# Optimization experiments

Hardware: AMD Instinct MI355X
Metric: run time of the kernel (lower is better)

The kernel has to match this reference:

```python
import jax
import jax.numpy as jnp
from jax import lax
import numpy as np

INPUT_DIM = 784
HIDDEN_DIM = 1024
BATCH = 256
N_BINS = 10


def setup_inputs() -> dict:
    key = jax.random.key(0)
    k1, k2, k3, k4, k5 = jax.random.split(key, 5)
    # kaiming-normal-ish init scales (faithful in spirit; exact values irrelevant for math)
    W = jax.random.normal(k1, (HIDDEN_DIM, INPUT_DIM), dtype=jnp.float32) * np.sqrt(2.0 / INPUT_DIM)
    c = jnp.zeros((HIDDEN_DIM, 1), dtype=jnp.float32)
    V = jax.random.normal(k2, (INPUT_DIM, HIDDEN_DIM, N_BINS), dtype=jnp.float32) * np.sqrt(2.0 / N_BINS)
    b = jnp.zeros((INPUT_DIM, N_BINS), dtype=jnp.float32)
    x = jax.random.randint(k3, (BATCH, INPUT_DIM), 0, N_BINS, dtype=jnp.int32)
    return {"x": x, "W": W, "c": c, "V": V, "b": b}


def reference(x, W, c, V, b):
    # x: [B, D] int pixel bins; W: [H, D]; c: [H, 1]; V: [D, H, 10]; b: [D, 10]
    B = x.shape[0]
    xf = x.astype(jnp.float32)  # [B, D]
    a0 = jnp.broadcast_to(c[:, 0][None, :], (B, W.shape[0]))  # [B, H]

    def step(a, inp):
        Vi, bi, Wi, xi = inp  # Vi:[H,10], bi:[10], Wi:[H], xi:[B]
        h = jax.nn.sigmoid(a)                       # [B, H]
        p = jax.nn.softmax(h @ Vi + bi, axis=1)     # [B, 10]
        a = a + xi[:, None] * Wi[None, :]           # rank-1 update, matches x_i @ W[:,i].T
        return a, p

    _, p_seq = lax.scan(step, a0, (V, b, W.T, xf.T))  # p_seq: [D, B, 10]
    p_hat = jnp.transpose(p_seq, (1, 2, 0))            # [B, 10, D] == torch.stack(p_hat, dim=2)
    return p_hat
```

## Files before the change

kernel.cpp:

```cpp
#include <hip/hip_runtime.h>
#include <stdint.h>

#define D_DIM 784
#define H_DIM 1024
#define B_DIM 256
#define NBIN  10
#define G_CH  8
#define T_CH  98
#define BT    16
#define BF    2
#define LOG2E 1.4426950408889634f

#define PSCAN_BLKS 256
#define VPREP_BLKS D_DIM
#define WPREP_BLKS 208

typedef _Float16 half8_t  __attribute__((ext_vector_type(8)));
typedef __fp16   fp16x2_t __attribute__((ext_vector_type(2)));
typedef float    float4_t __attribute__((ext_vector_type(4)));

__global__ void k_prep2(const float* __restrict__ W, const float* __restrict__ V,
                        const float* __restrict__ c, const int* __restrict__ x,
                        _Float16* __restrict__ Wt2h, _Float16* __restrict__ VB,
                        _Float16* __restrict__ PA) {
    __shared__ __align__(16) float smem[5120];
    int tid = threadIdx.x;
    int bx  = blockIdx.x;

    if (bx < PSCAN_BLKS) {
        int b0 = (bx & 127) * BF;
        int hg = bx >> 7;
        int h0 = hg * 512 + tid * 2;
        float* xs0 = smem;
        float* xs1 = smem + D_DIM;
        for (int qq = tid; qq < BF * (D_DIM / 4); qq += 256) {
            int bb = qq / (D_DIM / 4), r = qq % (D_DIM / 4);
            int4 xi = ((const int4*)(x + (size_t)(b0 + bb) * D_DIM))[r];
            float4 xf = make_float4((float)xi.x, (float)xi.y, (float)xi.z, (float)xi.w);
            *((float4*)((bb ? xs1 : xs0) + r * 4)) = xf;
        }
        float c0 = c[h0], c1 = c[h0 + 1];
        float acc00 = c0, acc01 = c1;
        float acc10 = c0, acc11 = c1;
        __syncthreads();
        const float4* w0 = (const float4*)(W + (size_t)h0 * D_DIM);
        const float4* w1 = (const float4*)(W + (size_t)(h0 + 1) * D_DIM);
        uint* pa0 = (uint*)PA + (size_t)b0 * (H_DIM / 2) + (h0 >> 1);

        auto pstore = [&](int t_) {
            union { _Float16 hh[2]; uint u; } u0, u1;
            u0.hh[0] = (_Float16)(acc00 * LOG2E); u0.hh[1] = (_Float16)(acc01 * LOG2E);
            u1.hh[0] = (_Float16)(acc10 * LOG2E); u1.hh[1] = (_Float16)(acc11 * LOG2E);
            pa0[(size_t)t_ * (B_DIM * H_DIM / 2)] = u0.u;
            pa0[(size_t)t_ * (B_DIM * H_DIM / 2) + (H_DIM / 2)] = u1.u;
        };
        auto pfma = [&](float4 a0_, float4 a1_, float4 b0_, float4 b1_, int t_) {
            float4 x00 = *((const float4*)(xs0 + t_ * 8));
            float4 x01 = *((const float4*)(xs0 + t_ * 8 + 4));
            float4 x10 = *((const float4*)(xs1 + t_ * 8));
            float4 x11 = *((const float4*)(xs1 + t_ * 8 + 4));
            acc00 += x00.x*a0_.x + x00.y*a0_.y + x00.z*a0_.z + x00.w*a0_.w
                   + x01.x*a1_.x + x01.y*a1_.y + x01.z*a1_.z + x01.w*a1_.w;
            acc01 += x00.x*b0_.x + x00.y*b0_.y + x00.z*b0_.z + x00.w*b0_.w
                   + x01.x*b1_.x + x01.y*b1_.y + x01.z*b1_.z + x01.w*b1_.w;
            acc10 += x10.x*a0_.x + x10.y*a0_.y + x10.z*a0_.z + x10.w*a0_.w
                   + x11.x*a1_.x + x11.y*a1_.y + x11.z*a1_.z + x11.w*a1_.w;
            acc11 += x10.x*b0_.x + x10.y*b0_.y + x10.z*b0_.z + x10.w*b0_.w
                   + x11.x*b1_.x + x11.y*b1_.y + x11.z*b1_.z + x11.w*b1_.w;
        };

        float4 A0 = w0[0], A1 = w0[1], B0 = w1[0], B1 = w1[1];
        for (int t = 0; t < T_CH; ++t) {
            int tn = (t + 1 < T_CH) ? t + 1 : t;
            float4 nA0 = w0[tn * 2], nA1 = w0[tn * 2 + 1];
            float4 nB0 = w1[tn * 2], nB1 = w1[tn * 2 + 1];
            pstore(t);
            pfma(A0, A1, B0, B1, t);
            A0 = nA0; A1 = nA1; B0 = nB0; B1 = nB1;
        }
    } else if (bx < PSCAN_BLKS + VPREP_BLKS) {
        int i = bx - PSCAN_BLKS;
        const float4* src = (const float4*)(V + (size_t)i * H_DIM * NBIN);
        uint4* dst = (uint4*)VB + (size_t)i * 2048;
        #pragma unroll
        for (int p = 0; p < 2; ++p) {
            if (p) __syncthreads();
            #pragma unroll
            for (int qv = 0; qv < 5; ++qv) {
                float4 v = src[p * 1280 + qv * 256 + tid];
                *((float4*)&smem[(qv * 256 + tid) * 4]) = v;
            }
            __syncthreads();
            #pragma unroll
            for (int qv = 0; qv < 4; ++qv) {
                int pair = p * 1024 + qv * 256 + tid;
                int kk = pair >> 6, ll = pair & 63;
                int n = ll & 15, hb = kk * 32 + ((ll >> 4) & 3) * 8;
                union { _Float16 hh[8]; uint4 u; } o;
                #pragma unroll
                for (int jj = 0; jj < 8; ++jj)
                    o.hh[jj] = (_Float16)((n < NBIN) ? smem[(hb + jj) * NBIN + n - p * 5120] : 0.0f);
                dst[pair] = o.u;
            }
        }
    } else {
        int qw = bx - PSCAN_BLKS - VPREP_BLKS;
        int j0 = (qw % 13) * 64, h0 = (qw / 13) * 64;
        float (*t)[65] = (float(*)[65])smem;
        int tj = tid & 63, tr = tid >> 6;
        int j = j0 + tj;
        #pragma unroll
        for (int r = 0; r < 16; ++r) {
            int hh = tr * 16 + r;
            t[hh][tj] = (j < D_DIM) ? W[(size_t)(h0 + hh) * D_DIM + j] : 0.0f;
        }
        __syncthreads();
        #pragma unroll
        for (int r = 0; r < 16; ++r) {
            int jj = tr * 16 + r;
            int jo = j0 + jj;
            if (jo < D_DIM) Wt2h[(size_t)jo * H_DIM + h0 + tj] = (_Float16)(t[tj][jj] * LOG2E);
        }
    }
}

__global__ __launch_bounds__(256, 4)
void k_main(const _Float16* __restrict__ VB, const _Float16* __restrict__ Wt2h,
            const _Float16* __restrict__ PA, const int* __restrict__ x,
            const float* __restrict__ bias, float* __restrict__ out) {
    int bt  = blockIdx.x;
    int tc  = blockIdx.y;
    int tid = threadIdx.x;
    int w   = tid >> 6;
    int l   = tid & 63;
    int bl  = l & 15;
    int kg  = l >> 4;
    int bg  = bt * BT + bl;
    int i0  = tc * G_CH;

    __shared__ __align__(16) _Float16 wlds[G_CH][H_DIM];
    __shared__ float red[4][64][18];
    __shared__ float bs[G_CH][16];

    {
        int ii = tid >> 4, n = tid & 15;
        if (ii < G_CH) bs[ii][n] = (n < NBIN) ? bias[(size_t)(i0 + ii) * NBIN + n] : 0.0f;
    }
    {
        #pragma unroll
        for (int r = 0; r < G_CH; ++r) {
            uint2 v = ((const uint2*)(Wt2h + (size_t)(i0 + r) * H_DIM))[tid];
            *((uint2*)&wlds[r][tid * 4]) = v;
        }
    }
    float xvf[G_CH];
    {
        const int4* xp = (const int4*)(x + (size_t)bg * D_DIM + i0);
        int4 x0 = xp[0], x1 = xp[1];
        xvf[0] = (float)x0.x; xvf[1] = (float)x0.y; xvf[2] = (float)x0.z; xvf[3] = (float)x0.w;
        xvf[4] = (float)x1.x; xvf[5] = (float)x1.y; xvf[6] = (float)x1.z; xvf[7] = (float)x1.w;
    }
    float a[8][8];
    {
        const _Float16* src = PA + ((size_t)tc * B_DIM + bg) * H_DIM + w * 256 + kg * 8;
        #pragma unroll
        for (int m = 0; m < 8; ++m) {
            half8_t av = *((const half8_t*)(src + m * 32));
            #pragma unroll
            for (int j = 0; j < 8; ++j) a[m][j] = (float)av[j];
        }
    }

    const uint4* vp = (const uint4*)VB + ((size_t)i0 * 32 + w * 8) * 64 + l;
    uint4 vbuf[3];
    vbuf[0] = vp[0];
    vbuf[1] = vp[64];
    float4_t acc = {0.f, 0.f, 0.f, 0.f};

    auto step = [&](int mm) {
        const int ii = mm >> 3, m = mm & 7;
        if (mm + 2 < 64) {
            const int nn = mm + 2;
            vbuf[nn % 3] = vp[((nn >> 3) * 32 + (nn & 7)) * 64];
        }
        union { half8_t h8; uint u32[4]; } af;
        #pragma unroll
        for (int p = 0; p < 4; ++p) {
            float s0 = __builtin_amdgcn_rcpf(1.0f + __builtin_amdgcn_exp2f(-a[m][2 * p]));
            float s1 = __builtin_amdgcn_rcpf(1.0f + __builtin_amdgcn_exp2f(-a[m][2 * p + 1]));
            union { fp16x2_t v; uint u; } cv;
            cv.v = __builtin_amdgcn_cvt_pkrtz(s0, s1);
            af.u32[p] = cv.u;
        }
        union { half8_t h8; uint4 u; } bf;
        bf.u = vbuf[mm % 3];
        acc = __builtin_amdgcn_mfma_f32_16x16x32_f16(af.h8, bf.h8, acc, 0, 0, 0);
        half8_t wh = *((const half8_t*)&wlds[ii][w * 256 + kg * 8 + m * 32]);
        float xf = xvf[ii];
        a[m][0] += xf * (float)wh[0]; a[m][1] += xf * (float)wh[1];
        a[m][2] += xf * (float)wh[2]; a[m][3] += xf * (float)wh[3];
        a[m][4] += xf * (float)wh[4]; a[m][5] += xf * (float)wh[5];
        a[m][6] += xf * (float)wh[6]; a[m][7] += xf * (float)wh[7];
        if (m == 7) {
            int s = (ii & 3) * 4;
            red[w][l][s + 0] = acc[0]; red[w][l][s + 1] = acc[1];
            red[w][l][s + 2] = acc[2]; red[w][l][s + 3] = acc[3];
            acc = (float4_t){0.f, 0.f, 0.f, 0.f};
        }
    };

    auto softmax_store = [&](int half) {
        float p4[4];
        #pragma unroll
        for (int q = 0; q < 4; ++q) {
            int ii = half * 4 + q;
            float tot = red[0][l][q * 4 + w] + red[1][l][q * 4 + w]
                      + red[2][l][q * 4 + w] + red[3][l][q * 4 + w];
            float v = (bl < NBIN) ? tot + bs[ii][bl] : -3.0e38f;
            float vm = v;
            vm = fmaxf(vm, __shfl_xor(vm, 1));
            vm = fmaxf(vm, __shfl_xor(vm, 2));
            vm = fmaxf(vm, __shfl_xor(vm, 4));
            vm = fmaxf(vm, __shfl_xor(vm, 8));
            float e = __builtin_amdgcn_exp2f((v - vm) * LOG2E);
            float ss = e;
            ss += __shfl_xor(ss, 1); ss += __shfl_xor(ss, 2);
            ss += __shfl_xor(ss, 4); ss += __shfl_xor(ss, 8);
            p4[q] = e * __builtin_amdgcn_rcpf(ss);
        }
        if (bl < NBIN) {
            int b = bt * BT + kg * 4 + w;
            size_t base = ((size_t)b * NBIN + bl) * D_DIM + i0 + half * 4;
            float4 v = make_float4(p4[0], p4[1], p4[2], p4[3]);
            *((float4*)(out + base)) = v;
        }
    };

    __syncthreads();
    #pragma unroll
    for (int mm = 0; mm < 32; ++mm) step(mm);
    __syncthreads();
    softmax_store(0);
    __syncthreads();
    #pragma unroll
    for (int mm = 32; mm < 64; ++mm) step(mm);
    __syncthreads();
    softmax_store(1);
}

extern "C" void kernel_launch(void* const* d_in, const int* in_sizes, int n_in,
                              void* d_out, int out_size, void* d_ws, size_t ws_size,
                              hipStream_t stream) {
    const int*   x    = (const int*)d_in[0];
    const float* W    = (const float*)d_in[1];
    const float* c    = (const float*)d_in[2];
    const float* V    = (const float*)d_in[3];
    const float* bias = (const float*)d_in[4];
    float* out = (float*)d_out;

    char* ws = (char*)d_ws;
    size_t off = 0;
    _Float16* Wt2h = (_Float16*)(ws + off);
    off += (size_t)D_DIM * H_DIM * sizeof(_Float16);
    off = (off + 255) & ~(size_t)255;
    _Float16* VB = (_Float16*)(ws + off);
    off += (size_t)D_DIM * 32 * 64 * 8 * sizeof(_Float16);
    off = (off + 255) & ~(size_t)255;
    _Float16* PA = (_Float16*)(ws + off);

    k_prep2<<<dim3(PSCAN_BLKS + VPREP_BLKS + WPREP_BLKS), 256, 0, stream>>>(W, V, c, x, Wt2h, VB, PA);
    k_main<<<dim3(B_DIM / BT, T_CH), 256, 0, stream>>>(VB, Wt2h, PA, x, bias, out);
}
```

Measured before the change: 219.4 us.

## Split prefix-scan prep across time groups with four batch rows per block

The prefix-sum prep blocks now handle four batch rows each and are split into four time-chunk groups, doubling the block count. Each block recomputes the prefix sums up to its chunk start and then emits about 25 checkpoints, buffering five steps in registers before storing. The aim is to shorten the long serial per-block loop of 98 steps and raise parallelism in the prep kernel. The cost is redundant prefix arithmetic in the later groups, more register pressure, and a different load balance against the V and W prep blocks.

```diff
diff --git a/kernel.cpp b/kernel.cpp
--- a/kernel.cpp
+++ b/kernel.cpp
@@ -8,10 +8,9 @@
 #define G_CH  8
 #define T_CH  98
 #define BT    16
-#define BF    2
 #define LOG2E 1.4426950408889634f
 
-#define PSCAN_BLKS 256
+#define PSCAN_BLKS 512
 #define VPREP_BLKS D_DIM
 #define WPREP_BLKS 208
 
@@ -28,55 +27,71 @@
     int bx  = blockIdx.x;
 
     if (bx < PSCAN_BLKS) {
-        int b0 = (bx & 127) * BF;
-        int hg = bx >> 7;
+        int bp = bx & 63;
+        int hg = (bx >> 6) & 1;
+        int tg = 3 - (bx >> 7);
+        int b0 = bp * 4;
         int h0 = hg * 512 + tid * 2;
-        float* xs0 = smem;
-        float* xs1 = smem + D_DIM;
-        for (int qq = tid; qq < BF * (D_DIM / 4); qq += 256) {
+        float (*xs)[D_DIM] = (float(*)[D_DIM])smem;
+        for (int qq = tid; qq < 4 * (D_DIM / 4); qq += 256) {
             int bb = qq / (D_DIM / 4), r = qq % (D_DIM / 4);
             int4 xi = ((const int4*)(x + (size_t)(b0 + bb) * D_DIM))[r];
-            float4 xf = make_float4((float)xi.x, (float)xi.y, (float)xi.z, (float)xi.w);
-            *((float4*)((bb ? xs1 : xs0) + r * 4)) = xf;
+            *((float4*)&xs[bb][r * 4]) =
+                make_float4((float)xi.x, (float)xi.y, (float)xi.z, (float)xi.w);
         }
         float c0 = c[h0], c1 = c[h0 + 1];
-        float acc00 = c0, acc01 = c1;
-        float acc10 = c0, acc11 = c1;
+        float a0[4], a1[4];
+        #pragma unroll
+        for (int b = 0; b < 4; ++b) { a0[b] = c0; a1[b] = c1; }
         __syncthreads();
         const float4* w0 = (const float4*)(W + (size_t)h0 * D_DIM);
         const float4* w1 = (const float4*)(W + (size_t)(h0 + 1) * D_DIM);
-        uint* pa0 = (uint*)PA + (size_t)b0 * (H_DIM / 2) + (h0 >> 1);
-
-        auto pstore = [&](int t_) {
-            union { _Float16 hh[2]; uint u; } u0, u1;
-            u0.hh[0] = (_Float16)(acc00 * LOG2E); u0.hh[1] = (_Float16)(acc01 * LOG2E);
-            u1.hh[0] = (_Float16)(acc10 * LOG2E); u1.hh[1] = (_Float16)(acc11 * LOG2E);
-            pa0[(size_t)t_ * (B_DIM * H_DIM / 2)] = u0.u;
-            pa0[(size_t)t_ * (B_DIM * H_DIM / 2) + (H_DIM / 2)] = u1.u;
+        uint* pau = (uint*)PA;
+        int hcol = hg * 256 + tid;
+        int t0 = tg * 25;
+
+        auto fma8 = [&](int t, float4 wa, float4 wb, float4 wc, float4 wd) {
+            #pragma unroll
+            for (int b = 0; b < 4; ++b) {
+                float4 xA = *((const float4*)&xs[b][t * 8]);
+                float4 xB = *((const float4*)&xs[b][t * 8 + 4]);
+                a0[b] += xA.x*wa.x + xA.y*wa.y + xA.z*wa.z + xA.w*wa.w
+                       + xB.x*wb.x + xB.y*wb.y + xB.z*wb.z + xB.w*wb.w;
+                a1[b] += xA.x*wc.x + xA.y*wc.y + xA.z*wc.z + xA.w*wc.w
+                       + xB.x*wd.x + xB.y*wd.y + xB.z*wd.z + xB.w*wd.w;
+            }
         };
-        auto pfma = [&](float4 a0_, float4 a1_, float4 b0_, float4 b1_, int t_) {
-            float4 x00 = *((const float4*)(xs0 + t_ * 8));
-            float4 x01 = *((const float4*)(xs0 + t_ * 8 + 4));
-            float4 x10 = *((const float4*)(xs1 + t_ * 8));
-            float4 x11 = *((const float4*)(xs1 + t_ * 8 + 4));
-            acc00 += x00.x*a0_.x + x00.y*a0_.y + x00.z*a0_.z + x00.w*a0_.w
-                   + x01.x*a1_.x + x01.y*a1_.y + x01.z*a1_.z + x01.w*a1_.w;
-            acc01 += x00.x*b0_.x + x00.y*b0_.y + x00.z*b0_.z + x00.w*b0_.w
-                   + x01.x*b1_.x + x01.y*b1_.y + x01.z*b1_.z + x01.w*b1_.w;
-            acc10 += x10.x*a0_.x + x10.y*a0_.y + x10.z*a0_.z + x10.w*a0_.w
-                   + x11.x*a1_.x + x11.y*a1_.y + x11.z*a1_.z + x11.w*a1_.w;
-            acc11 += x10.x*b0_.x + x10.y*b0_.y + x10.z*b0_.z + x10.w*b0_.w
-                   + x11.x*b1_.x + x11.y*b1_.y + x11.z*b1_.z + x11.w*b1_.w;
-        };
-
-        float4 A0 = w0[0], A1 = w0[1], B0 = w1[0], B1 = w1[1];
-        for (int t = 0; t < T_CH; ++t) {
-            int tn = (t + 1 < T_CH) ? t + 1 : t;
-            float4 nA0 = w0[tn * 2], nA1 = w0[tn * 2 + 1];
-            float4 nB0 = w1[tn * 2], nB1 = w1[tn * 2 + 1];
-            pstore(t);
-            pfma(A0, A1, B0, B1, t);
-            A0 = nA0; A1 = nA1; B0 = nB0; B1 = nB1;
+
+        #pragma unroll 2
+        for (int t = 0; t < t0; ++t)
+            fma8(t, w0[2*t], w0[2*t+1], w1[2*t], w1[2*t+1]);
+
+        #pragma unroll
+        for (int bo = 0; bo < 5; ++bo) {
+            uint chk[5][4];
+            #pragma unroll
+            for (int k = 0; k < 5; ++k) {
+                int t = t0 + bo * 5 + k;
+                if (t < T_CH) {
+                    #pragma unroll
+                    for (int b = 0; b < 4; ++b) {
+                        union { _Float16 hh[2]; uint u; } uu;
+                        uu.hh[0] = (_Float16)(a0[b] * LOG2E);
+                        uu.hh[1] = (_Float16)(a1[b] * LOG2E);
+                        chk[k][b] = uu.u;
+                    }
+                    fma8(t, w0[2*t], w0[2*t+1], w1[2*t], w1[2*t+1]);
+                }
+            }
+            #pragma unroll
+            for (int k = 0; k < 5; ++k) {
+                int t = t0 + bo * 5 + k;
+                if (t < T_CH) {
+                    #pragma unroll
+                    for (int b = 0; b < 4; ++b)
+                        pau[((size_t)t * B_DIM + b0 + b) * 512 + hcol] = chk[k][b];
+                }
+            }
         }
     } else if (bx < PSCAN_BLKS + VPREP_BLKS) {
         int i = bx - PSCAN_BLKS;
```

Result: slower. 251.3 us (+14.5%).

## Split prefix-scan into separate kernel reading transposed fp16 W

Applied to the files above, without the earlier changes.

The prefix accumulation of chunk-start activations moves out of the fused prep kernel into its own kernel, launched after the W transpose. It now reads the already-transposed, pre-scaled fp16 W with coalesced loads and uses one batch row per block over 512 blocks, instead of strided fp32 row reads over 256 blocks. This costs an extra kernel launch and serialises the scan behind the prep kernel rather than running alongside it. Accumulating with fp16 W instead of fp32 W also changes precision slightly.

```diff
diff --git a/kernel.cpp b/kernel.cpp
--- a/kernel.cpp
+++ b/kernel.cpp
@@ -8,10 +8,8 @@
 #define G_CH  8
 #define T_CH  98
 #define BT    16
-#define BF    2
 #define LOG2E 1.4426950408889634f
 
-#define PSCAN_BLKS 256
 #define VPREP_BLKS D_DIM
 #define WPREP_BLKS 208
 
@@ -19,67 +17,14 @@
 typedef __fp16   fp16x2_t __attribute__((ext_vector_type(2)));
 typedef float    float4_t __attribute__((ext_vector_type(4)));
 
-__global__ void k_prep2(const float* __restrict__ W, const float* __restrict__ V,
-                        const float* __restrict__ c, const int* __restrict__ x,
-                        _Float16* __restrict__ Wt2h, _Float16* __restrict__ VB,
-                        _Float16* __restrict__ PA) {
+__global__ void k_prep(const float* __restrict__ W, const float* __restrict__ V,
+                       _Float16* __restrict__ Wt2h, _Float16* __restrict__ VB) {
     __shared__ __align__(16) float smem[5120];
     int tid = threadIdx.x;
     int bx  = blockIdx.x;
 
-    if (bx < PSCAN_BLKS) {
-        int b0 = (bx & 127) * BF;
-        int hg = bx >> 7;
-        int h0 = hg * 512 + tid * 2;
-        float* xs0 = smem;
-        float* xs1 = smem + D_DIM;
-        for (int qq = tid; qq < BF * (D_DIM / 4); qq += 256) {
-            int bb = qq / (D_DIM / 4), r = qq % (D_DIM / 4);
-            int4 xi = ((const int4*)(x + (size_t)(b0 + bb) * D_DIM))[r];
-            float4 xf = make_float4((float)xi.x, (float)xi.y, (float)xi.z, (float)xi.w);
-            *((float4*)((bb ? xs1 : xs0) + r * 4)) = xf;
-        }
-        float c0 = c[h0], c1 = c[h0 + 1];
-        float acc00 = c0, acc01 = c1;
-        float acc10 = c0, acc11 = c1;
-        __syncthreads();
-        const float4* w0 = (const float4*)(W + (size_t)h0 * D_DIM);
-        const float4* w1 = (const float4*)(W + (size_t)(h0 + 1) * D_DIM);
-        uint* pa0 = (uint*)PA + (size_t)b0 * (H_DIM / 2) + (h0 >> 1);
-
-        auto pstore = [&](int t_) {
-            union { _Float16 hh[2]; uint u; } u0, u1;
-            u0.hh[0] = (_Float16)(acc00 * LOG2E); u0.hh[1] = (_Float16)(acc01 * LOG2E);
-            u1.hh[0] = (_Float16)(acc10 * LOG2E); u1.hh[1] = (_Float16)(acc11 * LOG2E);
-            pa0[(size_t)t_ * (B_DIM * H_DIM / 2)] = u0.u;
-            pa0[(size_t)t_ * (B_DIM * H_DIM / 2) + (H_DIM / 2)] = u1.u;
-        };
-        auto pfma = [&](float4 a0_, float4 a1_, float4 b0_, float4 b1_, int t_) {
-            float4 x00 = *((const float4*)(xs0 + t_ * 8));
-            float4 x01 = *((const float4*)(xs0 + t_ * 8 + 4));
-            float4 x10 = *((const float4*)(xs1 + t_ * 8));
-            float4 x11 = *((const float4*)(xs1 + t_ * 8 + 4));
-            acc00 += x00.x*a0_.x + x00.y*a0_.y + x00.z*a0_.z + x00.w*a0_.w
-                   + x01.x*a1_.x + x01.y*a1_.y + x01.z*a1_.z + x01.w*a1_.w;
-            acc01 += x00.x*b0_.x + x00.y*b0_.y + x00.z*b0_.z + x00.w*b0_.w
-                   + x01.x*b1_.x + x01.y*b1_.y + x01.z*b1_.z + x01.w*b1_.w;
-            acc10 += x10.x*a0_.x + x10.y*a0_.y + x10.z*a0_.z + x10.w*a0_.w
-                   + x11.x*a1_.x + x11.y*a1_.y + x11.z*a1_.z + x11.w*a1_.w;
-            acc11 += x10.x*b0_.x + x10.y*b0_.y + x10.z*b0_.z + x10.w*b0_.w
-                   + x11.x*b1_.x + x11.y*b1_.y + x11.z*b1_.z + x11.w*b1_.w;
-        };
-
-        float4 A0 = w0[0], A1 = w0[1], B0 = w1[0], B1 = w1[1];
-        for (int t = 0; t < T_CH; ++t) {
-            int tn = (t + 1 < T_CH) ? t + 1 : t;
-            float4 nA0 = w0[tn * 2], nA1 = w0[tn * 2 + 1];
-            float4 nB0 = w1[tn * 2], nB1 = w1[tn * 2 + 1];
-            pstore(t);
-            pfma(A0, A1, B0, B1, t);
-            A0 = nA0; A1 = nA1; B0 = nB0; B1 = nB1;
-        }
-    } else if (bx < PSCAN_BLKS + VPREP_BLKS) {
-        int i = bx - PSCAN_BLKS;
+    if (bx < VPREP_BLKS) {
+        int i = bx;
         const float4* src = (const float4*)(V + (size_t)i * H_DIM * NBIN);
         uint4* dst = (uint4*)VB + (size_t)i * 2048;
         #pragma unroll
@@ -104,7 +49,7 @@
             }
         }
     } else {
-        int qw = bx - PSCAN_BLKS - VPREP_BLKS;
+        int qw = bx - VPREP_BLKS;
         int j0 = (qw % 13) * 64, h0 = (qw / 13) * 64;
         float (*t)[65] = (float(*)[65])smem;
         int tj = tid & 63, tr = tid >> 6;
@@ -121,6 +66,59 @@
             int jo = j0 + jj;
             if (jo < D_DIM) Wt2h[(size_t)jo * H_DIM + h0 + tj] = (_Float16)(t[tj][jj] * LOG2E);
         }
+    }
+}
+
+__global__ __launch_bounds__(256)
+void k_pscan(const _Float16* __restrict__ Wt2h, const int* __restrict__ x,
+             const float* __restrict__ c, _Float16* __restrict__ PA) {
+    int b   = blockIdx.x;
+    int hg  = blockIdx.y;
+    int tid = threadIdx.x;
+    int hcol = hg * 256 + tid;
+    int h0   = hcol * 2;
+
+    __shared__ float xs[D_DIM];
+    if (tid < D_DIM / 4) {
+        int4 xi = ((const int4*)(x + (size_t)b * D_DIM))[tid];
+        *((float4*)&xs[tid * 4]) =
+            make_float4((float)xi.x, (float)xi.y, (float)xi.z, (float)xi.w);
+    }
+    float acc0 = c[h0] * LOG2E, acc1 = c[h0 + 1] * LOG2E;
+    __syncthreads();
+
+    const uint* wp  = (const uint*)Wt2h;
+    uint*       pau = (uint*)PA;
+
+    uint wvA[8], wvB[8];
+    auto ldrow = [&](int t, uint (&wv)[8]) {
+        #pragma unroll
+        for (int r = 0; r < 8; ++r)
+            wv[r] = wp[(size_t)(t * 8 + r) * 512 + hcol];
+    };
+    auto emit = [&](int t) {
+        union { _Float16 hh[2]; uint u; } uu;
+        uu.hh[0] = (_Float16)acc0; uu.hh[1] = (_Float16)acc1;
+        pau[((size_t)t * B_DIM + b) * 512 + hcol] = uu.u;
+    };
+    auto fmas = [&](int t, const uint (&wv)[8]) {
+        #pragma unroll
+        for (int r = 0; r < 8; ++r) {
+            union { uint u; _Float16 hh[2]; } uu; uu.u = wv[r];
+            float xf = xs[t * 8 + r];
+            acc0 += xf * (float)uu.hh[0];
+            acc1 += xf * (float)uu.hh[1];
+        }
+    };
+
+    ldrow(0, wvA);
+    for (int t = 0; t < T_CH; t += 2) {
+        ldrow(t + 1, wvB);
+        emit(t);
+        fmas(t, wvA);
+        if (t + 2 < T_CH) ldrow(t + 2, wvA);
+        emit(t + 1);
+        fmas(t + 1, wvB);
     }
 }
 
@@ -268,6 +266,7 @@
     off = (off + 255) & ~(size_t)255;
     _Float16* PA = (_Float16*)(ws + off);
 
-    k_prep2<<<dim3(PSCAN_BLKS + VPREP_BLKS + WPREP_BLKS), 256, 0, stream>>>(W, V, c, x, Wt2h, VB, PA);
+    k_prep<<<dim3(VPREP_BLKS + WPREP_BLKS), 256, 0, stream>>>(W, V, Wt2h, VB);
+    k_pscan<<<dim3(B_DIM, 2), 256, 0, stream>>>(Wt2h, x, c, PA);
     k_main<<<dim3(B_DIM / BT, T_CH), 256, 0, stream>>>(VB, Wt2h, PA, x, bias, out);
 }
```

New measurement: 191.9 us. 12.5% less time.
